# Optimization experiments

Measured on AMD Instinct MI355X. Metric: run time of the kernel, lower is better.

Reference implementation:

```python
import jax, jax.numpy as jnp
import numpy as np

H, W = 14, 14
HEAD_DIM = 32
HEADS = 24
HIDDEN = 768
RATE = 0.2
EPS = 1e-5


def _bias_idxs(h, w):
    # map_bias indexing: for flat pair index x over (h*w)^2
    x = jnp.arange(h * h * w * w)
    m, n = x // (h * w), x % (h * w)
    i, j = m // w, m % w
    ip, jp = n // w, n % w
    return (i - ip + h) * (2 * w) + (j - jp + w)


def _layer_norm(x, g, b):
    mu = jnp.mean(x, axis=-1, keepdims=True)
    var = jnp.mean(jnp.square(x - mu), axis=-1, keepdims=True)
    return (x - mu) * jax.lax.rsqrt(var + EPS) * g + b


def setup_inputs() -> dict:
    key = jax.random.key(0)
    ks = jax.random.split(key, 10)
    N, L = 64, H * W
    s = lambda fan_in: 1.0 / np.sqrt(fan_in)
    return {
        "x": jax.random.normal(ks[0], (N, L, HIDDEN), jnp.float32),
        "rel_bias": jax.random.uniform(ks[1], (1, 2 * H * 2 * W), jnp.float32, -0.5, 0.5),
        "wq": jax.random.normal(ks[2], (HEAD_DIM, HEAD_DIM), jnp.float32) * s(HEAD_DIM),
        "wk": jax.random.normal(ks[3], (HEAD_DIM, HEAD_DIM), jnp.float32) * s(HEAD_DIM),
        "wv": jax.random.normal(ks[4], (HEAD_DIM, HEAD_DIM), jnp.float32) * s(HEAD_DIM),
        "w_out": jax.random.normal(ks[5], (HIDDEN, HIDDEN), jnp.float32) * s(HIDDEN),
        "ln1_g": jnp.ones((HIDDEN,), jnp.float32),
        "ln1_b": jnp.zeros((HIDDEN,), jnp.float32),
        "ln2_g": jnp.ones((HIDDEN,), jnp.float32),
        "ln2_b": jnp.zeros((HIDDEN,), jnp.float32),
        "w1": jax.random.normal(ks[6], (4 * HIDDEN, HIDDEN), jnp.float32) * s(HIDDEN),
        "b1": jnp.zeros((4 * HIDDEN,), jnp.float32),
        "w2": jax.random.normal(ks[7], (HIDDEN, 4 * HIDDEN), jnp.float32) * s(4 * HIDDEN),
        "b2": jnp.zeros((HIDDEN,), jnp.float32),
    }


def reference(x, rel_bias, wq, wk, wv, w_out, ln1_g, ln1_b, ln2_g, ln2_b, w1, b1, w2, b2):
    N, L, _ = x.shape

    def attn(m):
        xh = m.reshape(N, L, HEADS, HEAD_DIM)
        # Linear(head_dim, head_dim) shared across heads; torch Linear: y = x @ W^T
        q = jnp.einsum("nlhd,ed->nlhe", xh, wq)
        k = jnp.einsum("nlhd,ed->nlhe", xh, wk)
        v = jnp.einsum("nlhd,ed->nlhe", xh, wv)
        scores = jnp.einsum("nqhd,nkhd->nhqk", q, k)
        bias = rel_bias[0][_bias_idxs(H, W)].reshape(1, 1, L, L)
        a = jax.nn.softmax((scores + bias) / np.sqrt(HEAD_DIM), axis=-1)
        o = jnp.einsum("nhqk,nkhd->nqhd", a, v).reshape(N, L, HIDDEN)
        return o @ w_out.T

    def ffn(m):
        h = jax.nn.gelu(m @ w1.T + b1, approximate=False)
        return h @ w2.T + b2

    # training-mode stochastic depth: deterministic scaling by RATE
    x = (x + attn(_layer_norm(x, ln1_g, ln1_b))) * RATE
    x = (x + ffn(_layer_norm(x, ln2_g, ln2_b))) * RATE
    return x
```

## Files before the change

### kernel.cpp

```cpp
#include <hip/hip_runtime.h>
#include <math.h>

#define NB    64
#define LSEQ  196
#define HID   768
#define NHEAD 24
#define HDIM  32
#define FFN   3072
#define ROWS  (NB * LSEQ)
#define RATE  0.2f
#define LN_EPS 1e-5f

typedef unsigned short bf16_t;
typedef short s16x8 __attribute__((ext_vector_type(8)));
typedef float f32x4 __attribute__((ext_vector_type(4)));

__device__ __forceinline__ unsigned short f2bf(float f) {
    unsigned u = __float_as_uint(f);
    unsigned r = u + 0x7fffu + ((u >> 16) & 1u);
    return (unsigned short)(r >> 16);
}

#define GLOAD_LDS16(g, l)                                                  \
    __builtin_amdgcn_global_load_lds(                                      \
        (const __attribute__((address_space(1))) void*)(g),                \
        (__attribute__((address_space(3))) void*)(l), 16, 0, 0)

#define WOUT4 (HID * HID / 4)
#define W14   (FFN * HID / 4)
__global__ __launch_bounds__(256) void cvt_w_kernel(
    const float* __restrict__ w_out, const float* __restrict__ w1,
    const float* __restrict__ w2, bf16_t* __restrict__ wob,
    bf16_t* __restrict__ w1b, bf16_t* __restrict__ w2b)
{
    int i = blockIdx.x * 256 + threadIdx.x;
    const float* src; bf16_t* dst; int off;
    if (i < WOUT4)            { src = w_out; dst = wob; off = i; }
    else if (i < WOUT4 + W14) { src = w1;    dst = w1b; off = i - WOUT4; }
    else                      { src = w2;    dst = w2b; off = i - WOUT4 - W14; }
    float4 v = ((const float4*)src)[off];
    uint2 p;
    p.x = (unsigned)f2bf(v.x) | ((unsigned)f2bf(v.y) << 16);
    p.y = (unsigned)f2bf(v.z) | ((unsigned)f2bf(v.w) << 16);
    ((uint2*)dst)[off] = p;
}

__global__ __launch_bounds__(256) void ln_kernel(
    const float* __restrict__ x, const float* __restrict__ g,
    const float* __restrict__ b, bf16_t* __restrict__ yv)
{
    int row = blockIdx.x;
    int tid = threadIdx.x;
    const float* xr = x + (size_t)row * HID;
    float v0 = xr[tid], v1 = xr[tid + 256], v2 = xr[tid + 512];
    __shared__ float rs[256], rs2[256];
    rs[tid]  = v0 + v1 + v2;
    rs2[tid] = v0 * v0 + v1 * v1 + v2 * v2;
    __syncthreads();
    for (int off = 128; off > 0; off >>= 1) {
        if (tid < off) { rs[tid] += rs[tid + off]; rs2[tid] += rs2[tid + off]; }
        __syncthreads();
    }
    float mean = rs[0] * (1.0f / HID);
    float var  = rs2[0] * (1.0f / HID) - mean * mean;
    float rstd = rsqrtf(var + LN_EPS);
    bf16_t* yr = yv + (size_t)row * HID;
    yr[tid]       = f2bf((v0 - mean) * rstd * g[tid]       + b[tid]);
    yr[tid + 256] = f2bf((v1 - mean) * rstd * g[tid + 256] + b[tid + 256]);
    yr[tid + 512] = f2bf((v2 - mean) * rstd * g[tid + 512] + b[tid + 512]);
}

__global__ __launch_bounds__(768) void ln_qkv_kernel(
    const float* __restrict__ x, const float* __restrict__ g,
    const float* __restrict__ b,
    const float* __restrict__ wq, const float* __restrict__ wk,
    const float* __restrict__ wv,
    bf16_t* __restrict__ q, bf16_t* __restrict__ k, bf16_t* __restrict__ v)
{
    int tid = threadIdx.x;
    int wv_ = tid >> 6, lane = tid & 63;
    __shared__ float wqs[32 * 33], wks[32 * 33], wvs[32 * 33];
    __shared__ float xs[HID];
    __shared__ float reds[12], reds2[12];
    for (int i = tid; i < 1024; i += 768) {
        int e = i >> 5, d = i & 31;
        wqs[e * 33 + d] = wq[i];
        wks[e * 33 + d] = wk[i];
        wvs[e * 33 + d] = wv[i];
    }
    int h = tid >> 5, e = tid & 31;
    float gg = g[tid], bb = b[tid];

    for (int rr = 0; rr < 4; rr++) {
        int row = blockIdx.x * 4 + rr;
        float xv = x[(size_t)row * HID + tid];
        float s = xv, s2 = xv * xv;
#pragma unroll
        for (int d = 32; d > 0; d >>= 1) {
            s  += __shfl_down(s, d);
            s2 += __shfl_down(s2, d);
        }
        __syncthreads();
        if (lane == 0) { reds[wv_] = s; reds2[wv_] = s2; }
        __syncthreads();
        float ts = 0.f, ts2 = 0.f;
#pragma unroll
        for (int i = 0; i < 12; i++) { ts += reds[i]; ts2 += reds2[i]; }
        float mean = ts * (1.0f / HID);
        float var  = ts2 * (1.0f / HID) - mean * mean;
        float rstd = rsqrtf(var + LN_EPS);
        xs[tid] = (xv - mean) * rstd * gg + bb;
        const float* xvp = xs + h * 32;
        float aq = 0.f, ak = 0.f, av = 0.f;
#pragma unroll
        for (int d = 0; d < 32; d++) {
            float xd = xvp[d];
            aq += xd * wqs[e * 33 + d];
            ak += xd * wks[e * 33 + d];
            av += xd * wvs[e * 33 + d];
        }
        size_t o = (size_t)row * HID + tid;
        q[o] = f2bf(aq); k[o] = f2bf(ak); v[o] = f2bf(av);
    }
}

#define VT_S 232
#define P_S  40

__global__ __launch_bounds__(256) void attn_mfma_kernel(
    const bf16_t* __restrict__ q, const bf16_t* __restrict__ k,
    const bf16_t* __restrict__ v, const float* __restrict__ rel_bias,
    bf16_t* __restrict__ o)
{
    int h = blockIdx.x;
    int n = blockIdx.y;
    int tid = threadIdx.x;
    int w = tid >> 6, lane = tid & 63;
    int lr = lane & 15;
    int lq = lane >> 4;

    __shared__ __align__(16) bf16_t Qs[208 * 32];
    __shared__ __align__(16) bf16_t Ks[224 * 32];
    __shared__ __align__(16) bf16_t Vt[32 * VT_S];
    __shared__ float bsh[28 * 28];
    __shared__ __align__(16) bf16_t Ps[4][16 * P_S];

    size_t base = (size_t)n * LSEQ * HID + (size_t)h * HDIM;

    for (int i = tid; i < 224 * 4; i += 256) {
        int r = i >> 2, c = i & 3;
        uint4 kv = make_uint4(0, 0, 0, 0);
        if (r < 196) kv = *(const uint4*)&k[base + (size_t)r * HID + c * 8];
        *(uint4*)&Ks[r * 32 + c * 8] = kv;
        if (r < 208) {
            uint4 qv = make_uint4(0, 0, 0, 0);
            if (r < 196) qv = *(const uint4*)&q[base + (size_t)r * HID + c * 8];
            *(uint4*)&Qs[r * 32 + c * 8] = qv;
        }
    }
    for (int i = tid; i < 196 * 16; i += 256) {
        int key = i >> 4, d2 = (i & 15) * 2;
        unsigned u = *(const unsigned*)&v[base + (size_t)key * HID + d2];
        Vt[d2 * VT_S + key]       = (bf16_t)(u & 0xffffu);
        Vt[(d2 + 1) * VT_S + key] = (bf16_t)(u >> 16);
    }
    for (int i = tid; i < 32 * 32; i += 256) {
        int d = i >> 5, kp = i & 31;
        if (kp < 28) Vt[d * VT_S + 196 + kp] = 0;
    }
    for (int i = tid; i < 784; i += 256) bsh[i] = rel_bias[i];
    __syncthreads();

    const float inv_sqrt_d = 0.17677669529663687f;
    bf16_t* P = Ps[w];

    for (int qt = w; qt < 13; qt += 4) {
        s16x8 aQ = *(const s16x8*)&Qs[(qt * 16 + lr) * 32 + lq * 8];

        int bb[4]; bool qvalid[4];
#pragma unroll
        for (int r = 0; r < 4; r++) {
            int qr = qt * 16 + lq * 4 + r;
            qvalid[r] = qr < LSEQ;
            int qq = qvalid[r] ? qr : 0;
            int qi = qq / 14, qj = qq - 14 * (qq / 14);
            bb[r] = (qi + 14) * 28 + (qj + 14);
        }

        f32x4 sf[14];
#pragma unroll
        for (int kt = 0; kt < 14; kt++) {
            s16x8 bK = *(const s16x8*)&Ks[(kt * 16 + lr) * 32 + lq * 8];
            f32x4 z = {};
            sf[kt] = __builtin_amdgcn_mfma_f32_16x16x32_bf16(aQ, bK, z, 0, 0, 0);
        }
#pragma unroll
        for (int kt = 0; kt < 14; kt++) {
            int key = kt * 16 + lr;
            bool kv = key < LSEQ;
            int kk2 = kv ? key : 0;
            int ip = kk2 / 14, jp = kk2 - 14 * ip;
            int boff = ip * 28 + jp;
#pragma unroll
            for (int r = 0; r < 4; r++) {
                float val = (sf[kt][r] + bsh[bb[r] - boff]) * inv_sqrt_d;
                sf[kt][r] = kv ? val : -1e30f;
            }
        }
        float mx[4];
#pragma unroll
        for (int r = 0; r < 4; r++) {
            float m = sf[0][r];
#pragma unroll
            for (int kt = 1; kt < 14; kt++) m = fmaxf(m, sf[kt][r]);
            mx[r] = m;
        }
#pragma unroll
        for (int d = 1; d < 16; d <<= 1)
#pragma unroll
            for (int r = 0; r < 4; r++)
                mx[r] = fmaxf(mx[r], __shfl_xor(mx[r], d));
        float sum[4] = {0.f, 0.f, 0.f, 0.f};
#pragma unroll
        for (int kt = 0; kt < 14; kt++)
#pragma unroll
            for (int r = 0; r < 4; r++) {
                float p = __expf(sf[kt][r] - mx[r]);
                sf[kt][r] = p;
                sum[r] += p;
            }
#pragma unroll
        for (int d = 1; d < 16; d <<= 1)
#pragma unroll
            for (int r = 0; r < 4; r++)
                sum[r] += __shfl_xor(sum[r], d);

        f32x4 oacc[2] = {};
#pragma unroll
        for (int kc = 0; kc < 7; kc++) {
#pragma unroll
            for (int r = 0; r < 4; r++) {
                P[(lq * 4 + r) * P_S + lr]      = f2bf(sf[2 * kc][r]);
                P[(lq * 4 + r) * P_S + 16 + lr] = f2bf(sf[2 * kc + 1][r]);
            }
            s16x8 aP = *(const s16x8*)&P[lr * P_S + lq * 8];
#pragma unroll
            for (int dt = 0; dt < 2; dt++) {
                s16x8 bV = *(const s16x8*)&Vt[(dt * 16 + lr) * VT_S + kc * 32 + lq * 8];
                oacc[dt] = __builtin_amdgcn_mfma_f32_16x16x32_bf16(aP, bV, oacc[dt], 0, 0, 0);
            }
        }
#pragma unroll
        for (int r = 0; r < 4; r++) {
            if (qvalid[r]) {
                float inv_l = 1.0f / sum[r];
                size_t ob = base + (size_t)(qt * 16 + lq * 4 + r) * HID;
                o[ob + lr]      = f2bf(oacc[0][r] * inv_l);
                o[ob + 16 + lr] = f2bf(oacc[1][r] * inv_l);
            }
        }
    }
}

__device__ __forceinline__ float gelu_exact(float x) {
    return 0.5f * x * (1.0f + erff(x * 0.70710678118654752f));
}

template <int MODE, bool OBF, int TM>
__global__ __launch_bounds__(256) void gemm_mfma(
    const bf16_t* __restrict__ A, const bf16_t* __restrict__ B,
    void* __restrict__ Cv, int M, int N, int K,
    const float* __restrict__ bias, const float* __restrict__ res, float scale)
{
    constexpr int MT = TM / 32;
    __shared__ __align__(16) bf16_t As[TM * 64];
    __shared__ __align__(16) bf16_t Bs[128 * 64];

    int tid = threadIdx.x;
    int mb = M / TM, nb = N >> 7;
    int gblk = blockIdx.x;
    int full = mb & ~7;
    int gfull = full * nb;
    int m_, n_;
    if (gblk < gfull) {
        int sg = gblk / (8 * nb), u = gblk - sg * (8 * nb);
        m_ = sg * 8 + (u & 7); n_ = u >> 3;
    } else {
        int u = gblk - gfull, rem = mb - full;
        m_ = full + u % rem; n_ = u / rem;
    }
    int bm = m_ * TM, bn = n_ << 7;

    int w    = tid >> 6;
    int lane = tid & 63;
    int wm = (w & 1) * (TM / 2);
    int wn = (w >> 1) * 64;
    int lr = lane & 15;
    int lq = lane >> 4;

    int srowl = lane >> 3;
    int scb   = ((lane & 7) ^ srowl) * 16;
    const char* Ab = (const char*)A;
    const char* Bb = (const char*)B;

    f32x4 acc[MT][4] = {};

    for (int k0 = 0; k0 < K; k0 += 64) {
#pragma unroll
        for (int j = 0; j < TM / 32; j++) {
            int rb = w * (TM / 4) + j * 8;
            GLOAD_LDS16(Ab + ((size_t)(bm + rb + srowl) * K + k0) * 2 + scb, &As[rb * 64]);
        }
#pragma unroll
        for (int j = 0; j < 4; j++) {
            int rb = w * 32 + j * 8;
            GLOAD_LDS16(Bb + ((size_t)(bn + rb + srowl) * K + k0) * 2 + scb, &Bs[rb * 64]);
        }
        __syncthreads();

        int sw = lr & 7;
#pragma unroll
        for (int kc = 0; kc < 2; kc++) {
            int cof = (((kc << 2) | lq) ^ sw) * 8;
            s16x8 af[MT], bf[4];
#pragma unroll
            for (int t = 0; t < MT; t++)
                af[t] = *(const s16x8*)&As[(wm + t * 16 + lr) * 64 + cof];
#pragma unroll
            for (int t = 0; t < 4; t++)
                bf[t] = *(const s16x8*)&Bs[(wn + t * 16 + lr) * 64 + cof];
#pragma unroll
            for (int tm = 0; tm < MT; tm++)
#pragma unroll
                for (int tn = 0; tn < 4; tn++)
                    acc[tm][tn] = __builtin_amdgcn_mfma_f32_16x16x32_bf16(
                        af[tm], bf[tn], acc[tm][tn], 0, 0, 0);
        }
        __syncthreads();
    }

#pragma unroll
    for (int tm = 0; tm < MT; tm++) {
#pragma unroll
        for (int tn = 0; tn < 4; tn++) {
#pragma unroll
            for (int r = 0; r < 4; r++) {
                int mrow = bm + wm + tm * 16 + lq * 4 + r;
                int ncol = bn + wn + tn * 16 + lr;
                float vacc = acc[tm][tn][r];
                if (MODE == 1) {
                    vacc = (res[(size_t)mrow * N + ncol] + vacc) * scale;
                } else if (MODE == 2) {
                    vacc = gelu_exact(vacc + bias[ncol]);
                } else if (MODE == 3) {
                    vacc = (res[(size_t)mrow * N + ncol] + vacc + bias[ncol]) * scale;
                }
                if (OBF) ((bf16_t*)Cv)[(size_t)mrow * N + ncol] = f2bf(vacc);
                else     ((float*)Cv)[(size_t)mrow * N + ncol] = vacc;
            }
        }
    }
}

extern "C" void kernel_launch(void* const* d_in, const int* in_sizes, int n_in,
                              void* d_out, int out_size, void* d_ws, size_t ws_size,
                              hipStream_t stream)
{
    const float* x        = (const float*)d_in[0];
    const float* rel_bias = (const float*)d_in[1];
    const float* wq       = (const float*)d_in[2];
    const float* wk       = (const float*)d_in[3];
    const float* wv       = (const float*)d_in[4];
    const float* w_out    = (const float*)d_in[5];
    const float* ln1_g    = (const float*)d_in[6];
    const float* ln1_b    = (const float*)d_in[7];
    const float* ln2_g    = (const float*)d_in[8];
    const float* ln2_b    = (const float*)d_in[9];
    const float* w1       = (const float*)d_in[10];
    const float* b1       = (const float*)d_in[11];
    const float* w2       = (const float*)d_in[12];
    const float* b2       = (const float*)d_in[13];
    float* out = (float*)d_out;
    float* ws  = (float*)d_ws;

    const size_t SZ = (size_t)ROWS * HID;
    bf16_t* q_bf = (bf16_t*)(ws + SZ);
    bf16_t* k_bf = (bf16_t*)(ws + 2 * SZ);
    bf16_t* v_bf = (bf16_t*)(ws + 3 * SZ);
    bf16_t* o_bf = (bf16_t*)ws;
    bf16_t* y2b  = (bf16_t*)(ws + SZ / 2);
    bf16_t* h    = (bf16_t*)(ws + SZ);
    bf16_t* wob  = (bf16_t*)(ws + 4 * SZ);
    bf16_t* w1b  = wob + (size_t)HID * HID;
    bf16_t* w2b  = w1b + (size_t)FFN * HID;

    cvt_w_kernel<<<(WOUT4 + 2 * W14 + 255) / 256, 256, 0, stream>>>(
        w_out, w1, w2, wob, w1b, w2b);

    ln_qkv_kernel<<<ROWS / 4, 768, 0, stream>>>(x, ln1_g, ln1_b, wq, wk, wv,
                                                q_bf, k_bf, v_bf);

    attn_mfma_kernel<<<dim3(NHEAD, NB), 256, 0, stream>>>(q_bf, k_bf, v_bf, rel_bias, o_bf);

    gemm_mfma<1, false, 64><<<(ROWS / 64) * (HID / 128), 256, 0, stream>>>(
        o_bf, wob, out, ROWS, HID, HID, nullptr, x, RATE);

    ln_kernel<<<ROWS, 256, 0, stream>>>(out, ln2_g, ln2_b, y2b);

    gemm_mfma<2, true, 128><<<(ROWS / 128) * (FFN / 128), 256, 0, stream>>>(
        y2b, w1b, h, ROWS, FFN, HID, b1, nullptr, 1.0f);

    gemm_mfma<3, false, 64><<<(ROWS / 64) * (HID / 128), 256, 0, stream>>>(
        h, w2b, out, ROWS, HID, FFN, b2, out, RATE);
}
```

Baseline: 532.8 us.

## Compute fused LayerNorm+QKV projection with bf16 MFMA on 16-row tiles

Replaces the scalar per-thread 32-wide dot products for Q/K/V with MFMA 16x16x32 bf16 instructions. Each block now handles 16 rows, one wavefront per row, and LayerNorm uses wavefront shuffle reductions with float4 loads instead of block-wide shared reductions. The normalized input is staged as bf16 in shared memory before the matmul, which reduces the precision of the projection input. Output stores are 16-lane scattered 2-byte writes, which may coalesce poorly.

```diff
diff --git a/kernel.cpp b/kernel.cpp
--- a/kernel.cpp
+++ b/kernel.cpp
@@ -70,7 +70,8 @@
     yr[tid + 512] = f2bf((v2 - mean) * rstd * g[tid + 512] + b[tid + 512]);
 }
 
-__global__ __launch_bounds__(768) void ln_qkv_kernel(
+#define QKV_T 16
+__global__ __launch_bounds__(256) void ln_qkv_mfma_kernel(
     const float* __restrict__ x, const float* __restrict__ g,
     const float* __restrict__ b,
     const float* __restrict__ wq, const float* __restrict__ wk,
@@ -78,49 +79,94 @@
     bf16_t* __restrict__ q, bf16_t* __restrict__ k, bf16_t* __restrict__ v)
 {
     int tid = threadIdx.x;
-    int wv_ = tid >> 6, lane = tid & 63;
-    __shared__ float wqs[32 * 33], wks[32 * 33], wvs[32 * 33];
-    __shared__ float xs[HID];
-    __shared__ float reds[12], reds2[12];
-    for (int i = tid; i < 1024; i += 768) {
-        int e = i >> 5, d = i & 31;
-        wqs[e * 33 + d] = wq[i];
-        wks[e * 33 + d] = wk[i];
-        wvs[e * 33 + d] = wv[i];
-    }
-    int h = tid >> 5, e = tid & 31;
-    float gg = g[tid], bb = b[tid];
-
-    for (int rr = 0; rr < 4; rr++) {
-        int row = blockIdx.x * 4 + rr;
-        float xv = x[(size_t)row * HID + tid];
-        float s = xv, s2 = xv * xv;
-#pragma unroll
-        for (int d = 32; d > 0; d >>= 1) {
-            s  += __shfl_down(s, d);
-            s2 += __shfl_down(s2, d);
-        }
-        __syncthreads();
-        if (lane == 0) { reds[wv_] = s; reds2[wv_] = s2; }
-        __syncthreads();
-        float ts = 0.f, ts2 = 0.f;
-#pragma unroll
-        for (int i = 0; i < 12; i++) { ts += reds[i]; ts2 += reds2[i]; }
-        float mean = ts * (1.0f / HID);
-        float var  = ts2 * (1.0f / HID) - mean * mean;
-        float rstd = rsqrtf(var + LN_EPS);
-        xs[tid] = (xv - mean) * rstd * gg + bb;
-        const float* xvp = xs + h * 32;
-        float aq = 0.f, ak = 0.f, av = 0.f;
-#pragma unroll
-        for (int d = 0; d < 32; d++) {
-            float xd = xvp[d];
-            aq += xd * wqs[e * 33 + d];
-            ak += xd * wks[e * 33 + d];
-            av += xd * wvs[e * 33 + d];
-        }
-        size_t o = (size_t)row * HID + tid;
-        q[o] = f2bf(aq); k[o] = f2bf(ak); v[o] = f2bf(av);
+    int w = tid >> 6, lane = tid & 63;
+    int lr = lane & 15, lq = lane >> 4;
+
+    __shared__ __align__(16) bf16_t Xs[QKV_T * 24 * 32];
+    __shared__ __align__(16) bf16_t Wqs[32 * 32];
+    __shared__ __align__(16) bf16_t Wks[32 * 32];
+    __shared__ __align__(16) bf16_t Wvs[32 * 32];
+
+    for (int i = tid; i < 1024; i += 256) {
+        Wqs[i] = f2bf(wq[i]);
+        Wks[i] = f2bf(wk[i]);
+        Wvs[i] = f2bf(wv[i]);
+    }
+
+    float4 gv[3], bv[3];
+#pragma unroll
+    for (int i = 0; i < 3; i++) {
+        gv[i] = ((const float4*)g)[lane + i * 64];
+        bv[i] = ((const float4*)b)[lane + i * 64];
+    }
+
+    for (int j = 0; j < 4; j++) {
+        int lt = w * 4 + j;
+        size_t row = (size_t)blockIdx.x * QKV_T + lt;
+        const float4* xr = (const float4*)(x + row * HID);
+        float4 xv[3];
+        float s = 0.f, s2 = 0.f;
+#pragma unroll
+        for (int i = 0; i < 3; i++) {
+            xv[i] = xr[lane + i * 64];
+            s  += xv[i].x + xv[i].y + xv[i].z + xv[i].w;
+            s2 += xv[i].x * xv[i].x + xv[i].y * xv[i].y
+                + xv[i].z * xv[i].z + xv[i].w * xv[i].w;
+        }
+#pragma unroll
+        for (int d = 1; d < 64; d <<= 1) {
+            s  += __shfl_xor(s, d);
+            s2 += __shfl_xor(s2, d);
+        }
+        float mean = s * (1.0f / HID);
+        float rstd = rsqrtf(s2 * (1.0f / HID) - mean * mean + LN_EPS);
+#pragma unroll
+        for (int i = 0; i < 3; i++) {
+            int idx  = (lane + i * 64) * 4;
+            int head = idx >> 5, d0 = idx & 31;
+            float o0 = (xv[i].x - mean) * rstd * gv[i].x + bv[i].x;
+            float o1 = (xv[i].y - mean) * rstd * gv[i].y + bv[i].y;
+            float o2 = (xv[i].z - mean) * rstd * gv[i].z + bv[i].z;
+            float o3 = (xv[i].w - mean) * rstd * gv[i].w + bv[i].w;
+            uint2 p;
+            p.x = (unsigned)f2bf(o0) | ((unsigned)f2bf(o1) << 16);
+            p.y = (unsigned)f2bf(o2) | ((unsigned)f2bf(o3) << 16);
+            *(uint2*)&Xs[(lt * 24 + head) * 32 + d0] = p;
+        }
+    }
+    __syncthreads();
+
+    s16x8 bq[2], bk[2], bvv[2];
+    bq[0]  = *(const s16x8*)&Wqs[lr * 32 + lq * 8];
+    bq[1]  = *(const s16x8*)&Wqs[(16 + lr) * 32 + lq * 8];
+    bk[0]  = *(const s16x8*)&Wks[lr * 32 + lq * 8];
+    bk[1]  = *(const s16x8*)&Wks[(16 + lr) * 32 + lq * 8];
+    bvv[0] = *(const s16x8*)&Wvs[lr * 32 + lq * 8];
+    bvv[1] = *(const s16x8*)&Wvs[(16 + lr) * 32 + lq * 8];
+
+    for (int t = 0; t < 6; t++) {
+        int tile = w * 6 + t;
+        s16x8 aX = *(const s16x8*)&Xs[(tile * 16 + lr) * 32 + lq * 8];
+        f32x4 z = {};
+        f32x4 aq0 = __builtin_amdgcn_mfma_f32_16x16x32_bf16(aX, bq[0],  z, 0, 0, 0);
+        f32x4 aq1 = __builtin_amdgcn_mfma_f32_16x16x32_bf16(aX, bq[1],  z, 0, 0, 0);
+        f32x4 ak0 = __builtin_amdgcn_mfma_f32_16x16x32_bf16(aX, bk[0],  z, 0, 0, 0);
+        f32x4 ak1 = __builtin_amdgcn_mfma_f32_16x16x32_bf16(aX, bk[1],  z, 0, 0, 0);
+        f32x4 av0 = __builtin_amdgcn_mfma_f32_16x16x32_bf16(aX, bvv[0], z, 0, 0, 0);
+        f32x4 av1 = __builtin_amdgcn_mfma_f32_16x16x32_bf16(aX, bvv[1], z, 0, 0, 0);
+        int rbase = tile * 16 + lq * 4;
+#pragma unroll
+        for (int r = 0; r < 4; r++) {
+            int xrow = rbase + r;
+            int t_loc = xrow / 24, head = xrow - t_loc * 24;
+            size_t gb = ((size_t)blockIdx.x * QKV_T + t_loc) * HID + head * 32;
+            q[gb + lr]      = f2bf(aq0[r]);
+            q[gb + 16 + lr] = f2bf(aq1[r]);
+            k[gb + lr]      = f2bf(ak0[r]);
+            k[gb + 16 + lr] = f2bf(ak1[r]);
+            v[gb + lr]      = f2bf(av0[r]);
+            v[gb + 16 + lr] = f2bf(av1[r]);
+        }
     }
 }
 
@@ -397,8 +443,8 @@
     cvt_w_kernel<<<(WOUT4 + 2 * W14 + 255) / 256, 256, 0, stream>>>(
         w_out, w1, w2, wob, w1b, w2b);
 
-    ln_qkv_kernel<<<ROWS / 4, 768, 0, stream>>>(x, ln1_g, ln1_b, wq, wk, wv,
-                                                q_bf, k_bf, v_bf);
+    ln_qkv_mfma_kernel<<<ROWS / QKV_T, 256, 0, stream>>>(
+        x, ln1_g, ln1_b, wq, wk, wv, q_bf, k_bf, v_bf);
 
     attn_mfma_kernel<<<dim3(NHEAD, NB), 256, 0, stream>>>(q_bf, k_bf, v_bf, rel_bias, o_bf);
 
```

Result: faster. 454.8 us (-14.6%).
